# Kernel tuning notes

Measured on AMD Instinct MI355X. Metric: run time of the kernel, lower is better.

The kernel has to match this reference:

```python
import jax, jax.numpy as jnp
import numpy as np

NNODES = 6144
DIM = 64
LAYERS = 3
K = 24
ALPHA = 3.0


def setup_inputs() -> dict:
    key = jax.random.key(0)
    ks = jax.random.split(key, 8)
    lin_scale = 1.0 / np.sqrt(DIM)
    return {
        "idx": jnp.arange(NNODES, dtype=jnp.int64) if jax.config.jax_enable_x64 else jnp.arange(NNODES, dtype=jnp.int32),
        "scale_idx": 1,
        "scale_set": jax.random.uniform(ks[0], (LAYERS,), dtype=jnp.float32),
        "emb1": jax.random.normal(ks[1], (NNODES, DIM), dtype=jnp.float32),
        "emb2": jax.random.normal(ks[2], (NNODES, DIM), dtype=jnp.float32),
        "W1": jax.random.uniform(ks[3], (LAYERS, DIM, DIM), dtype=jnp.float32, minval=-lin_scale, maxval=lin_scale),
        "b1": jax.random.uniform(ks[4], (LAYERS, DIM), dtype=jnp.float32, minval=-lin_scale, maxval=lin_scale),
        "W2": jax.random.uniform(ks[5], (LAYERS, DIM, DIM), dtype=jnp.float32, minval=-lin_scale, maxval=lin_scale),
        "b2": jax.random.uniform(ks[6], (LAYERS, DIM), dtype=jnp.float32, minval=-lin_scale, maxval=lin_scale),
    }


def reference(idx, scale_idx, scale_set, emb1, emb2, W1, b1, W2, b2):
    # idx: [N] node ids; scale_idx unused (as in the original forward body)
    n = idx.shape[0]
    nodevec1 = emb1[idx]  # [N, D]
    nodevec2 = emb2[idx]  # [N, D]
    rows = jnp.arange(n)[:, None]  # [N, 1] row indices for scatter
    adj_set = []
    for i in range(LAYERS):
        # per-layer tanh MLP update (state carried across layers)
        nodevec1 = jnp.tanh(ALPHA * ((nodevec1 * scale_set[i]) @ W1[i].T + b1[i]))
        nodevec2 = jnp.tanh(ALPHA * ((nodevec2 * scale_set[i]) @ W2[i].T + b2[i]))
        # antisymmetric similarity: [N, N]
        a = nodevec1 @ nodevec2.T - nodevec2 @ nodevec1.T
        adj0 = jax.nn.relu(jnp.tanh(ALPHA * a))
        # topk per row -> binary mask (scatter of constant 1, matching s1.fill_(1))
        _, t1 = jax.lax.top_k(adj0, K)  # t1: [N, K]
        mask = jnp.zeros((n, n), dtype=adj0.dtype).at[rows, t1].set(1.0)
        adj_set.append(adj0 * mask)
    return jnp.stack(adj_set)  # [LAYERS, N, N]
```

## Files before the change

### kernel.cpp

```cpp
#include <hip/hip_runtime.h>
#include <hip/hip_bf16.h>

#define NN 6144
#define DD 64
#define NL 3
#define KK 24
#define BT 64
#define KH 32
#define MB 4
#define KCLAMP 7.99881172180175781f
#define BANDLO 6.5f

typedef unsigned long long ull;

__device__ __forceinline__ float tanh_xla(float x) {
  float xc = fminf(fmaxf(x, -KCLAMP), KCLAMP);
  float x2 = xc * xc;
  float p = -2.76076847742355e-16f;
  p = fmaf(p, x2, 2.00018790482477e-13f);
  p = fmaf(p, x2, -8.60467152213735e-11f);
  p = fmaf(p, x2, 5.12229709037114e-08f);
  p = fmaf(p, x2, 1.48572235717979e-05f);
  p = fmaf(p, x2, 6.37261928875436e-04f);
  p = fmaf(p, x2, 4.89352455891786e-03f);
  p = xc * p;
  float q = 1.19825839466702e-06f;
  q = fmaf(q, x2, 1.18534705686654e-04f);
  q = fmaf(q, x2, 2.26843463243900e-03f);
  q = fmaf(q, x2, 4.89352518554385e-03f);
  float r = p / q;
  return (fabsf(x) < 0.0004f) ? x : r;
}

__device__ __forceinline__ ull shfl_xor_u64(ull v, int m) {
  unsigned lo = __shfl_xor((unsigned)v, m);
  unsigned hi = __shfl_xor((unsigned)(v >> 32), m);
  return ((ull)hi << 32) | lo;
}

__global__ __launch_bounds__(256) void mlp_kernel(
    const int* __restrict__ idx, const float* __restrict__ scale_set,
    const float* __restrict__ emb1, const float* __restrict__ emb2,
    const float* __restrict__ W1, const float* __restrict__ b1,
    const float* __restrict__ W2, const float* __restrict__ b2,
    float* __restrict__ vt1, float* __restrict__ vt2) {
  __shared__ float Wt1[DD][DD];
  __shared__ float Wt2[DD][DD];
  __shared__ float bsh1[DD], bsh2[DD];
  __shared__ __align__(16) float o1sh[MB][DD];
  __shared__ __align__(16) float o2sh[MB][DD];
  const int t = threadIdx.x;
  const int r = t >> 6;
  const int j = t & 63;
  const int grow = blockIdx.x * MB + r;

  {
    int g = idx[grow];
    if (j < 16) {
      ((float4*)&o1sh[r][0])[j] = ((const float4*)(emb1 + (size_t)g * DD))[j];
      ((float4*)&o2sh[r][0])[j] = ((const float4*)(emb2 + (size_t)g * DD))[j];
    }
  }

  for (int l = 0; l < NL; ++l) {
    __syncthreads();
    {
      const float* w1p = W1 + ((size_t)l * DD + j) * DD + r * 16;
      const float* w2p = W2 + ((size_t)l * DD + j) * DD + r * 16;
#pragma unroll
      for (int w = 0; w < 4; ++w) {
        float4 a = *(const float4*)(w1p + 4 * w);
        float4 b = *(const float4*)(w2p + 4 * w);
        int k0 = r * 16 + 4 * w;
        Wt1[k0 + 0][j] = a.x; Wt1[k0 + 1][j] = a.y;
        Wt1[k0 + 2][j] = a.z; Wt1[k0 + 3][j] = a.w;
        Wt2[k0 + 0][j] = b.x; Wt2[k0 + 1][j] = b.y;
        Wt2[k0 + 2][j] = b.z; Wt2[k0 + 3][j] = b.w;
      }
    }
    if (t < DD) { bsh1[t] = b1[l * DD + t]; bsh2[t] = b2[l * DD + t]; }
    __syncthreads();

    const float s = scale_set[l];
    float a1 = 0.0f, a2 = 0.0f;
#pragma unroll
    for (int kb = 0; kb < 16; ++kb) {
      float4 s1 = ((const float4*)&o1sh[r][0])[kb];
      float4 s2 = ((const float4*)&o2sh[r][0])[kb];
      int k0 = 4 * kb;
      a1 = fmaf(s1.x * s, Wt1[k0 + 0][j], a1);
      a1 = fmaf(s1.y * s, Wt1[k0 + 1][j], a1);
      a1 = fmaf(s1.z * s, Wt1[k0 + 2][j], a1);
      a1 = fmaf(s1.w * s, Wt1[k0 + 3][j], a1);
      a2 = fmaf(s2.x * s, Wt2[k0 + 0][j], a2);
      a2 = fmaf(s2.y * s, Wt2[k0 + 1][j], a2);
      a2 = fmaf(s2.z * s, Wt2[k0 + 2][j], a2);
      a2 = fmaf(s2.w * s, Wt2[k0 + 3][j], a2);
    }
    float t1 = tanh_xla(3.0f * (a1 + bsh1[j]));
    float t2 = tanh_xla(3.0f * (a2 + bsh2[j]));
    __syncthreads();
    o1sh[r][j] = t1;
    o2sh[r][j] = t2;
    vt1[((size_t)l * DD + j) * NN + grow] = t1;
    vt2[((size_t)l * DD + j) * NN + grow] = t2;
  }
}

__global__ __launch_bounds__(128) void xmat_kernel(
    const float* __restrict__ vt1, const float* __restrict__ vt2,
    float* __restrict__ out) {
  __shared__ float R1h[KH][BT];
  __shared__ float R2h[KH][BT];
  __shared__ float C1h[KH][BT];
  __shared__ float C2h[KH][BT];

  const int a = blockIdx.x;
  const int b = blockIdx.y;
  if (b < a) return;
  const int l = blockIdx.z;
  const int t = threadIdx.x;
  const int r0 = a * BT;
  const int c0 = b * BT;
  const float* w1 = vt1 + (size_t)l * DD * NN;
  const float* w2 = vt2 + (size_t)l * DD * NN;
  float* o = out + (size_t)l * NN * NN;

  const int ty = t >> 3;
  const int tx = t & 7;
  const int stk = t >> 4;
  const int stc = (t & 15) * 4;

  float acc1[4][8] = {{0.f}}, acc2[4][8] = {{0.f}};

#pragma unroll
  for (int h = 0; h < 2; ++h) {
    __syncthreads();
#pragma unroll
    for (int m = 0; m < 4; ++m) {
      int k = m * 8 + stk;
      const size_t src = (size_t)(h * KH + k) * NN;
      *(float4*)&R1h[k][stc] = *(const float4*)(w1 + src + r0 + stc);
      *(float4*)&R2h[k][stc] = *(const float4*)(w2 + src + r0 + stc);
      *(float4*)&C1h[k][stc] = *(const float4*)(w1 + src + c0 + stc);
      *(float4*)&C2h[k][stc] = *(const float4*)(w2 + src + c0 + stc);
    }
    __syncthreads();
#pragma unroll 4
    for (int kk = 0; kk < KH; ++kk) {
      float4 rv1 = *(const float4*)&R1h[kk][4 * ty];
      float4 rv2 = *(const float4*)&R2h[kk][4 * ty];
      float4 cv1a = *(const float4*)&C1h[kk][8 * tx];
      float4 cv1b = *(const float4*)&C1h[kk][8 * tx + 4];
      float4 cv2a = *(const float4*)&C2h[kk][8 * tx];
      float4 cv2b = *(const float4*)&C2h[kk][8 * tx + 4];
      const float* r1 = (const float*)&rv1;
      const float* r2 = (const float*)&rv2;
      float c1[8], c2[8];
      *(float4*)&c1[0] = cv1a; *(float4*)&c1[4] = cv1b;
      *(float4*)&c2[0] = cv2a; *(float4*)&c2[4] = cv2b;
#pragma unroll
      for (int i = 0; i < 4; ++i)
#pragma unroll
        for (int j = 0; j < 8; ++j) {
          acc1[i][j] = fmaf(r1[i], c2[j], acc1[i][j]);
          acc2[i][j] = fmaf(r2[i], c1[j], acc2[i][j]);
        }
    }
  }

#pragma unroll
  for (int i = 0; i < 4; ++i) {
    float4 xa, xb;
    xa.x = 3.0f * (acc1[i][0] - acc2[i][0]);
    xa.y = 3.0f * (acc1[i][1] - acc2[i][1]);
    xa.z = 3.0f * (acc1[i][2] - acc2[i][2]);
    xa.w = 3.0f * (acc1[i][3] - acc2[i][3]);
    xb.x = 3.0f * (acc1[i][4] - acc2[i][4]);
    xb.y = 3.0f * (acc1[i][5] - acc2[i][5]);
    xb.z = 3.0f * (acc1[i][6] - acc2[i][6]);
    xb.w = 3.0f * (acc1[i][7] - acc2[i][7]);
    float* p = o + (size_t)(r0 + 4 * ty + i) * NN + c0 + 8 * tx;
    *(float4*)p = xa;
    *(float4*)(p + 4) = xb;
  }
  if (b > a) {
#pragma unroll
    for (int j = 0; j < 8; ++j) {
      float4 xt;
      xt.x = 3.0f * (acc2[0][j] - acc1[0][j]);
      xt.y = 3.0f * (acc2[1][j] - acc1[1][j]);
      xt.z = 3.0f * (acc2[2][j] - acc1[2][j]);
      xt.w = 3.0f * (acc2[3][j] - acc1[3][j]);
      *(float4*)(o + (size_t)(c0 + 8 * tx + j) * NN + r0 + 4 * ty) = xt;
    }
  }
}

__global__ __launch_bounds__(256, 4) void topk_kernel(float* __restrict__ out) {
  const int t = threadIdx.x;
  const int w = t >> 6;
  const int lane = t & 63;
  const int row = blockIdx.x * 4 + w;
  float* rp = out + (size_t)row * NN;
  const float Rclamp = tanh_xla(8.0f);
  const unsigned RB = __float_as_uint(Rclamp);
  const ull KOFF = 1ull << 62;
  const ull RKEYHI = (ull)RB << 32;
  const double EMPTYD = __longlong_as_double((long long)KOFF);

  ull mlo = 0ull, mhi = 0ull;
  double s[KK];
#pragma unroll
  for (int q = 0; q < KK; ++q) s[q] = EMPTYD;
  ull s0k = KOFF;
  unsigned plat_total = 0;

  float4 cur = *(const float4*)(rp + (size_t)lane * 4);
  for (int sb = 0; sb < 24; ++sb) {
    float4 nxt = cur;
    if (sb < 23) nxt = *(const float4*)(rp + (size_t)((sb + 1) * 64 + lane) * 4);
    const float* xp = (const float*)&cur;
    const unsigned gbase = (unsigned)(sb * 256 + lane * 4);

    bool p0 = cur.x >= KCLAMP, p1 = cur.y >= KCLAMP,
         p2 = cur.z >= KCLAMP, p3 = cur.w >= KCLAMP;
    unsigned nib = (p0 ? 1u : 0u) | (p1 ? 2u : 0u) | (p2 ? 4u : 0u) | (p3 ? 8u : 0u);

    if (plat_total < 24) {
      plat_total += (unsigned)__popcll(__ballot(p0));
      plat_total += (unsigned)__popcll(__ballot(p1));
      plat_total += (unsigned)__popcll(__ballot(p2));
      plat_total += (unsigned)__popcll(__ballot(p3));
#pragma unroll
      for (int jj = 0; jj < 4; ++jj) {
        float x = xp[jj];
        if (x > 0.0f && x < KCLAMP) {
          float tv = tanh_xla(x);
          ull key = KOFF | ((ull)__float_as_uint(tv) << 32) |
                    (ull)(0xFFFFu - (gbase + jj));
          if (key > s0k) {
            double kd = __longlong_as_double((long long)key);
#pragma unroll
            for (int i = 0; i < KK - 1; ++i)
              s[i] = fmin(s[i + 1], fmax(s[i], kd));
            s[KK - 1] = fmax(s[KK - 1], kd);
            s0k = (ull)__double_as_longlong(s[0]);
          }
        }
      }
    } else {
      bool b0 = (cur.x > BANDLO) & !p0, b1 = (cur.y > BANDLO) & !p1,
           b2 = (cur.z > BANDLO) & !p2, b3 = (cur.w > BANDLO) & !p3;
      if (__any(b0 | b1 | b2 | b3)) {
#pragma unroll
        for (int jj = 0; jj < 4; ++jj) {
          bool bj = (jj == 0) ? b0 : (jj == 1) ? b1 : (jj == 2) ? b2 : b3;
          if (bj) {
            float tv = tanh_xla(xp[jj]);
            unsigned tvb = __float_as_uint(tv);
            if (tvb > RB) {
              ull key = KOFF | ((ull)tvb << 32) | (ull)(0xFFFFu - (gbase + jj));
              if (key > s0k) {
                double kd = __longlong_as_double((long long)key);
#pragma unroll
                for (int i = 0; i < KK - 1; ++i)
                  s[i] = fmin(s[i + 1], fmax(s[i], kd));
                s[KK - 1] = fmax(s[KK - 1], kd);
                s0k = (ull)__double_as_longlong(s[0]);
              }
            } else if (tvb == RB) {
              nib |= 1u << jj;
            }
          }
        }
      }
    }
    if (sb < 16) mlo |= ((ull)nib) << (sb * 4);
    else         mhi |= ((ull)nib) << ((sb - 16) * 4);
    cur = nxt;
  }

  float wv = 0.0f;
  int wi = 0;
  for (int r = 0; r < KK; ++r) {
    ull pk = KOFF;
    if (mlo | mhi) {
      int e = mlo ? __builtin_ctzll(mlo) : (64 + __builtin_ctzll(mhi));
      int pidx = ((e >> 2) << 8) + lane * 4 + (e & 3);
      pk = KOFF | RKEYHI | (ull)(0xFFFFu - (unsigned)pidx);
    }
    ull lk = (ull)__double_as_longlong(s[KK - 1]);
    bool fromList = lk > pk;
    ull cand = fromList ? lk : pk;
    ull win = cand;
#pragma unroll
    for (int d = 1; d < 64; d <<= 1) {
      ull o2 = shfl_xor_u64(win, d);
      win = (o2 > win) ? o2 : win;
    }
    if (win == KOFF) break;
    if (lane == r) {
      wv = __uint_as_float((unsigned)((win >> 32) & 0x3FFFFFFFu));
      wi = 0xFFFF - (int)(win & 0xFFFFull);
    }
    if (cand == win) {
      if (fromList) {
#pragma unroll
        for (int i = KK - 1; i > 0; --i) s[i] = s[i - 1];
        s[0] = EMPTYD;
      } else {
        if (mlo) mlo &= mlo - 1;
        else     mhi &= mhi - 1;
      }
    }
  }

  float4 z = make_float4(0.f, 0.f, 0.f, 0.f);
  for (int sb = 0; sb < 24; ++sb)
    *(float4*)(rp + (size_t)(sb * 64 + lane) * 4) = z;
  asm volatile("s_waitcnt vmcnt(0)" ::: "memory");
  if (wv > 0.0f) rp[wi] = wv;
}

extern "C" void kernel_launch(void* const* d_in, const int* in_sizes, int n_in,
                              void* d_out, int out_size, void* d_ws, size_t ws_size,
                              hipStream_t stream) {
  const int*   idx       = (const int*)d_in[0];
  const float* scale_set = (const float*)d_in[2];
  const float* emb1      = (const float*)d_in[3];
  const float* emb2      = (const float*)d_in[4];
  const float* W1        = (const float*)d_in[5];
  const float* b1        = (const float*)d_in[6];
  const float* W2        = (const float*)d_in[7];
  const float* b2        = (const float*)d_in[8];
  float* out = (float*)d_out;

  const size_t VS = (size_t)NL * NN * DD;
  float* vt1 = (float*)d_ws;
  float* vt2 = vt1 + VS;

  mlp_kernel<<<NN / MB, 256, 0, stream>>>(idx, scale_set, emb1, emb2, W1, b1, W2, b2,
                                          vt1, vt2);
  xmat_kernel<<<dim3(NN / BT, NN / BT, NL), 128, 0, stream>>>(vt1, vt2, out);
  topk_kernel<<<(NL * NN) / 4, 256, 0, stream>>>(out);
}
```

Measured before the change: 736.3 us.

## Add fast path in top-k for rows saturated with clamp-valued entries

```diff
diff --git a/kernel.cpp b/kernel.cpp
--- a/kernel.cpp
+++ b/kernel.cpp
@@ -197,7 +197,7 @@
   }
 }
 
-__global__ __launch_bounds__(256, 4) void topk_kernel(float* __restrict__ out) {
+__global__ __launch_bounds__(256, 2) void topk_kernel(float* __restrict__ out) {
   const int t = threadIdx.x;
   const int w = t >> 6;
   const int lane = t & 63;
@@ -205,37 +205,100 @@
   float* rp = out + (size_t)row * NN;
   const float Rclamp = tanh_xla(8.0f);
   const unsigned RB = __float_as_uint(Rclamp);
-  const ull KOFF = 1ull << 62;
-  const ull RKEYHI = (ull)RB << 32;
-  const double EMPTYD = __longlong_as_double((long long)KOFF);
-
-  ull mlo = 0ull, mhi = 0ull;
-  double s[KK];
-#pragma unroll
-  for (int q = 0; q < KK; ++q) s[q] = EMPTYD;
-  ull s0k = KOFF;
-  unsigned plat_total = 0;
+  const ull lmask = (1ull << lane) - 1;
+
+  ull wlo = 0ull, whi = 0ull;
+  unsigned T = 0;
+  bool flag = false;
 
   float4 cur = *(const float4*)(rp + (size_t)lane * 4);
   for (int sb = 0; sb < 24; ++sb) {
     float4 nxt = cur;
     if (sb < 23) nxt = *(const float4*)(rp + (size_t)((sb + 1) * 64 + lane) * 4);
-    const float* xp = (const float*)&cur;
-    const unsigned gbase = (unsigned)(sb * 256 + lane * 4);
 
     bool p0 = cur.x >= KCLAMP, p1 = cur.y >= KCLAMP,
          p2 = cur.z >= KCLAMP, p3 = cur.w >= KCLAMP;
-    unsigned nib = (p0 ? 1u : 0u) | (p1 ? 2u : 0u) | (p2 ? 4u : 0u) | (p3 ? 8u : 0u);
-
-    if (plat_total < 24) {
-      plat_total += (unsigned)__popcll(__ballot(p0));
-      plat_total += (unsigned)__popcll(__ballot(p1));
-      plat_total += (unsigned)__popcll(__ballot(p2));
-      plat_total += (unsigned)__popcll(__ballot(p3));
+    unsigned rbnib = (p0 ? 1u : 0u) | (p1 ? 2u : 0u) |
+                     (p2 ? 4u : 0u) | (p3 ? 8u : 0u);
+
+    bool b0 = (cur.x > BANDLO) & !p0, b1 = (cur.y > BANDLO) & !p1,
+         b2 = (cur.z > BANDLO) & !p2, b3 = (cur.w > BANDLO) & !p3;
+    if (__any(b0 | b1 | b2 | b3)) {
+      if (b0) { unsigned v = __float_as_uint(tanh_xla(cur.x));
+                if (v == RB) rbnib |= 1u; else if (v > RB) flag = true; }
+      if (b1) { unsigned v = __float_as_uint(tanh_xla(cur.y));
+                if (v == RB) rbnib |= 2u; else if (v > RB) flag = true; }
+      if (b2) { unsigned v = __float_as_uint(tanh_xla(cur.z));
+                if (v == RB) rbnib |= 4u; else if (v > RB) flag = true; }
+      if (b3) { unsigned v = __float_as_uint(tanh_xla(cur.w));
+                if (v == RB) rbnib |= 8u; else if (v > RB) flag = true; }
+    }
+
+    if (T < 24u) {
+      ull bl0 = __ballot((rbnib & 1u) != 0u);
+      ull bl1 = __ballot((rbnib & 2u) != 0u);
+      ull bl2 = __ballot((rbnib & 4u) != 0u);
+      ull bl3 = __ballot((rbnib & 8u) != 0u);
+      unsigned below = (unsigned)__popcll(bl0 & lmask) +
+                       (unsigned)__popcll(bl1 & lmask) +
+                       (unsigned)__popcll(bl2 & lmask) +
+                       (unsigned)__popcll(bl3 & lmask);
+      unsigned base = T + below;
+#pragma unroll
+      for (int jj = 0; jj < 4; ++jj) {
+        if (rbnib & (1u << jj)) {
+          unsigned rk = base + (unsigned)__builtin_popcount(rbnib & ((1u << jj) - 1u));
+          if (rk < 24u) {
+            if (sb < 16) wlo |= 1ull << (sb * 4 + jj);
+            else         whi |= 1ull << ((sb - 16) * 4 + jj);
+          }
+        }
+      }
+      T += (unsigned)__popcll(bl0) + (unsigned)__popcll(bl1) +
+           (unsigned)__popcll(bl2) + (unsigned)__popcll(bl3);
+    }
+    cur = nxt;
+  }
+
+  if (T >= 24u && !__any(flag)) {
+    float4 z = make_float4(0.f, 0.f, 0.f, 0.f);
+    for (int sb = 0; sb < 24; ++sb)
+      *(float4*)(rp + (size_t)(sb * 64 + lane) * 4) = z;
+    asm volatile("s_waitcnt vmcnt(0)" ::: "memory");
+    while (wlo) {
+      int e = __builtin_ctzll(wlo);
+      rp[(e >> 2) * 256 + lane * 4 + (e & 3)] = Rclamp;
+      wlo &= wlo - 1;
+    }
+    while (whi) {
+      int e = __builtin_ctzll(whi);
+      rp[(16 + (e >> 2)) * 256 + lane * 4 + (e & 3)] = Rclamp;
+      whi &= whi - 1;
+    }
+    return;
+  }
+
+  {
+    const ull KOFF = 1ull << 62;
+    const ull RKEYHI = (ull)RB << 32;
+    const double EMPTYD = __longlong_as_double((long long)KOFF);
+    ull mlo = 0ull, mhi = 0ull;
+    double s[KK];
+#pragma unroll
+    for (int q = 0; q < KK; ++q) s[q] = EMPTYD;
+    ull s0k = KOFF;
+
+    for (int sb = 0; sb < 24; ++sb) {
+      float4 x4 = *(const float4*)(rp + (size_t)(sb * 64 + lane) * 4);
+      const float* xp = (const float*)&x4;
+      const unsigned gbase = (unsigned)(sb * 256 + lane * 4);
+      unsigned nib = 0u;
 #pragma unroll
       for (int jj = 0; jj < 4; ++jj) {
         float x = xp[jj];
-        if (x > 0.0f && x < KCLAMP) {
+        if (x >= KCLAMP) {
+          nib |= 1u << jj;
+        } else if (x > 0.0f) {
           float tv = tanh_xla(x);
           ull key = KOFF | ((ull)__float_as_uint(tv) << 32) |
                     (ull)(0xFFFFu - (gbase + jj));
@@ -249,78 +312,51 @@
           }
         }
       }
-    } else {
-      bool b0 = (cur.x > BANDLO) & !p0, b1 = (cur.y > BANDLO) & !p1,
-           b2 = (cur.z > BANDLO) & !p2, b3 = (cur.w > BANDLO) & !p3;
-      if (__any(b0 | b1 | b2 | b3)) {
-#pragma unroll
-        for (int jj = 0; jj < 4; ++jj) {
-          bool bj = (jj == 0) ? b0 : (jj == 1) ? b1 : (jj == 2) ? b2 : b3;
-          if (bj) {
-            float tv = tanh_xla(xp[jj]);
-            unsigned tvb = __float_as_uint(tv);
-            if (tvb > RB) {
-              ull key = KOFF | ((ull)tvb << 32) | (ull)(0xFFFFu - (gbase + jj));
-              if (key > s0k) {
-                double kd = __longlong_as_double((long long)key);
-#pragma unroll
-                for (int i = 0; i < KK - 1; ++i)
-                  s[i] = fmin(s[i + 1], fmax(s[i], kd));
-                s[KK - 1] = fmax(s[KK - 1], kd);
-                s0k = (ull)__double_as_longlong(s[0]);
-              }
-            } else if (tvb == RB) {
-              nib |= 1u << jj;
-            }
-          }
+      if (sb < 16) mlo |= ((ull)nib) << (sb * 4);
+      else         mhi |= ((ull)nib) << ((sb - 16) * 4);
+    }
+
+    float wv = 0.0f;
+    int wi = 0;
+    for (int r = 0; r < KK; ++r) {
+      ull pk = KOFF;
+      if (mlo | mhi) {
+        int e = mlo ? __builtin_ctzll(mlo) : (64 + __builtin_ctzll(mhi));
+        int pidx = ((e >> 2) << 8) + lane * 4 + (e & 3);
+        pk = KOFF | RKEYHI | (ull)(0xFFFFu - (unsigned)pidx);
+      }
+      ull lk = (ull)__double_as_longlong(s[KK - 1]);
+      bool fromList = lk > pk;
+      ull cand = fromList ? lk : pk;
+      ull win = cand;
+#pragma unroll
+      for (int d = 1; d < 64; d <<= 1) {
+        ull o2 = shfl_xor_u64(win, d);
+        win = (o2 > win) ? o2 : win;
+      }
+      if (win == KOFF) break;
+      if (lane == r) {
+        wv = __uint_as_float((unsigned)((win >> 32) & 0x3FFFFFFFu));
+        wi = 0xFFFF - (int)(win & 0xFFFFull);
+      }
+      if (cand == win) {
+        if (fromList) {
+#pragma unroll
+          for (int i = KK - 1; i > 0; --i) s[i] = s[i - 1];
+          s[0] = EMPTYD;
+        } else {
+          if (mlo) mlo &= mlo - 1;
+          else     mhi &= mhi - 1;
         }
       }
     }
-    if (sb < 16) mlo |= ((ull)nib) << (sb * 4);
-    else         mhi |= ((ull)nib) << ((sb - 16) * 4);
-    cur = nxt;
-  }
-
-  float wv = 0.0f;
-  int wi = 0;
-  for (int r = 0; r < KK; ++r) {
-    ull pk = KOFF;
-    if (mlo | mhi) {
-      int e = mlo ? __builtin_ctzll(mlo) : (64 + __builtin_ctzll(mhi));
-      int pidx = ((e >> 2) << 8) + lane * 4 + (e & 3);
-      pk = KOFF | RKEYHI | (ull)(0xFFFFu - (unsigned)pidx);
-    }
-    ull lk = (ull)__double_as_longlong(s[KK - 1]);
-    bool fromList = lk > pk;
-    ull cand = fromList ? lk : pk;
-    ull win = cand;
-#pragma unroll
-    for (int d = 1; d < 64; d <<= 1) {
-      ull o2 = shfl_xor_u64(win, d);
-      win = (o2 > win) ? o2 : win;
-    }
-    if (win == KOFF) break;
-    if (lane == r) {
-      wv = __uint_as_float((unsigned)((win >> 32) & 0x3FFFFFFFu));
-      wi = 0xFFFF - (int)(win & 0xFFFFull);
-    }
-    if (cand == win) {
-      if (fromList) {
-#pragma unroll
-        for (int i = KK - 1; i > 0; --i) s[i] = s[i - 1];
-        s[0] = EMPTYD;
-      } else {
-        if (mlo) mlo &= mlo - 1;
-        else     mhi &= mhi - 1;
-      }
-    }
-  }
-
-  float4 z = make_float4(0.f, 0.f, 0.f, 0.f);
-  for (int sb = 0; sb < 24; ++sb)
-    *(float4*)(rp + (size_t)(sb * 64 + lane) * 4) = z;
-  asm volatile("s_waitcnt vmcnt(0)" ::: "memory");
-  if (wv > 0.0f) rp[wi] = wv;
+
+    float4 z = make_float4(0.f, 0.f, 0.f, 0.f);
+    for (int sb = 0; sb < 24; ++sb)
+      *(float4*)(rp + (size_t)(sb * 64 + lane) * 4) = z;
+    asm volatile("s_waitcnt vmcnt(0)" ::: "memory");
+    if (wv > 0.0f) rp[wi] = wv;
+  }
 }
 
 extern "C" void kernel_launch(void* const* d_in, const int* in_sizes, int n_in,
```

Result: faster. 658.1 us (-10.6%).
